# Optimization experiments

Measured on AMD Instinct MI355X. Metric: run time of the kernel, lower is better.

Reference implementation:

```python
import jax, jax.numpy as jnp
import numpy as np

B, S, D = 4, 2048, 512
H, Dh = 8, 64  # head_dim(=num heads)=8, qkv_dim(per-head)=64
SCALE = 1.0 / float(np.sqrt(Dh))


def setup_inputs() -> dict:
    key = jax.random.key(0)
    ks = jax.random.split(key, 11)
    w = 1.0 / float(np.sqrt(D))
    return {
        "x": jax.random.normal(ks[0], (B, S, D), dtype=jnp.float32),
        "mask": jax.random.randint(ks[1], (B, 1, S, S), 0, 2, dtype=jnp.int32),
        "Wq": jax.random.normal(ks[2], (D, H * Dh), dtype=jnp.float32) * w,
        "bq": jax.random.normal(ks[3], (H * Dh,), dtype=jnp.float32) * w,
        "Wk": jax.random.normal(ks[4], (D, H * Dh), dtype=jnp.float32) * w,
        "bk": jax.random.normal(ks[5], (H * Dh,), dtype=jnp.float32) * w,
        "Wv": jax.random.normal(ks[6], (D, H * Dh), dtype=jnp.float32) * w,
        "bv": jax.random.normal(ks[7], (H * Dh,), dtype=jnp.float32) * w,
        "Wo": jax.random.normal(ks[8], (H * Dh, D), dtype=jnp.float32) * w,
        "bo": jax.random.normal(ks[9], (D,), dtype=jnp.float32) * w,
    }


def reference(x, mask, Wq, bq, Wk, bk, Wv, bv, Wo, bo):
    b = x.shape[0]
    q = (x @ Wq + bq).reshape(b, S, H, Dh)
    k = (x @ Wk + bk).reshape(b, S, H, Dh)
    v = (x @ Wv + bv).reshape(b, S, H, Dh)
    # [b,h,q,k] attention scores, softmax over k
    score = jax.nn.softmax(jnp.einsum('bqhd,bkhd->bhqk', q, k) * SCALE, axis=-1)
    # faithful quirk: mask applied AFTER softmax, masked entries set to 1e-20
    score = jnp.where(mask == 1, jnp.float32(1e-20), score)
    # faithful quirk: einsum 'bvhd,bhqk->bvhd' sums score over q AND k -> [b,h] scalar per head
    s = score.sum(axis=(-2, -1))  # [b, h]
    att = v * s[:, None, :, None]  # [b, S, H, Dh]
    out = att.reshape(b, S, H * Dh) @ Wo + bo
    return out
```

## Files before the change

### kernel.cpp

```cpp
#include <hip/hip_runtime.h>
#include <cstdint>
#include <cstddef>

#define DEVINL __device__ __forceinline__

constexpr int S_ = 2048;
constexpr int D_ = 512;
constexpr int H_ = 8;
constexpr float SCALE_ = 0.125f;
constexpr float SCALE_L2E_ = 0.18033688011112f;

using short8 = __attribute__((ext_vector_type(8))) short;
using f32x4  = __attribute__((ext_vector_type(4))) float;

DEVINL unsigned short f2bf(float f){
  unsigned u = __builtin_bit_cast(unsigned, f);
  u += 0x7FFFu + ((u >> 16) & 1u);
  return (unsigned short)(u >> 16);
}
DEVINL float bf2f(unsigned short h){
  return __builtin_bit_cast(float, ((unsigned)h) << 16);
}

DEVINL float fast_exp2(float x){ return __builtin_amdgcn_exp2f(x); }

DEVINL void gload16(const void* g, void* l){
  __builtin_amdgcn_global_load_lds(
      (__attribute__((address_space(1))) void*)(g),
      (__attribute__((address_space(3))) void*)(l), 16, 0, 0);
}

__global__ __launch_bounds__(256) void prep_kernel(
    const float* __restrict__ x, unsigned short* __restrict__ xb,
    const int* __restrict__ mask, unsigned char* __restrict__ bits,
    const float* __restrict__ W0, const float* __restrict__ W1,
    const float* __restrict__ W2, const float* __restrict__ W3,
    unsigned short* __restrict__ WT)
{
  __shared__ float tile[32][33];
  const int bid = blockIdx.x, t = threadIdx.x;
  if (bid < 2048){
    int i = bid * 256 + t;
    const float* p = x + (size_t)i * 8;
    float4 a = *(const float4*)p;
    float4 b = *(const float4*)(p + 4);
    short8 o;
    o[0]=f2bf(a.x); o[1]=f2bf(a.y); o[2]=f2bf(a.z); o[3]=f2bf(a.w);
    o[4]=f2bf(b.x); o[5]=f2bf(b.y); o[6]=f2bf(b.z); o[7]=f2bf(b.w);
    *(short8*)(xb + (size_t)i*8) = o;
  } else if (bid < 4096){
    unsigned tid = (bid - 2048) * 256 + t;
    #pragma unroll
    for (int it = 0; it < 4; ++it){
      size_t bidx = (size_t)tid + (size_t)it * 524288;
      const int* p = mask + bidx * 8;
      int4 a = *(const int4*)p;
      int4 c = *(const int4*)(p + 4);
      unsigned v = (unsigned)(a.x != 0)       | ((unsigned)(a.y != 0) << 1)
                 | ((unsigned)(a.z != 0) << 2) | ((unsigned)(a.w != 0) << 3)
                 | ((unsigned)(c.x != 0) << 4) | ((unsigned)(c.y != 0) << 5)
                 | ((unsigned)(c.z != 0) << 6) | ((unsigned)(c.w != 0) << 7);
      bits[bidx] = (unsigned char)v;
    }
  } else {
    const int b2 = bid - 4096;
    const int z = b2 >> 8, r = b2 & 255;
    const float* W = (z==0) ? W0 : (z==1 ? W1 : (z==2 ? W2 : W3));
    const float scale = (z==0) ? SCALE_L2E_ : 1.0f;
    unsigned short* out = WT + (size_t)z * D_ * D_;
    const int n0 = (r & 15)*32, k0 = (r >> 4)*32;
    const int tx = t & 31, ty = t >> 5;
    #pragma unroll
    for (int j=0;j<4;j++)
      tile[ty+j*8][tx] = W[(size_t)(k0+ty+j*8)*D_ + n0+tx];
    __syncthreads();
    #pragma unroll
    for (int j=0;j<4;j++)
      out[(size_t)(n0+ty+j*8)*D_ + k0+tx] = f2bf(tile[tx][ty+j*8]*scale);
  }
}

template<typename OutT>
__global__ __launch_bounds__(256) void gemm_bt(
    const unsigned short* __restrict__ A, long long Az,
    const unsigned short* __restrict__ BT, long long Bz,
    const float* __restrict__ bias0, const float* __restrict__ bias1, const float* __restrict__ bias2,
    float bs0, float bs1, float bs2,
    OutT* __restrict__ Cp, long long Cz)
{
  __shared__ unsigned short As[128*64];
  __shared__ unsigned short Bs[128*64];
  const int z = blockIdx.z;
  const unsigned short* Ab = A + (size_t)z*Az;
  const unsigned short* Bb = BT + (size_t)z*Bz;
  const float* bias = (z==0) ? bias0 : (z==1 ? bias1 : bias2);
  const float bscale = (z==0) ? bs0 : (z==1 ? bs1 : bs2);
  OutT* C = Cp + (size_t)z*Cz;
  const int m0 = blockIdx.y*128, n0 = blockIdx.x*128;
  const int t = threadIdx.x, lane = t & 63, w = t >> 6;
  const int wr = w >> 1, wc = w & 1;
  const int g = lane >> 4, lq = lane & 15;
  f32x4 acc[4][4] = {};
  for (int kk = 0; kk < D_; kk += 64){
    #pragma unroll
    for (int p = 0; p < 4; p++){
      int o = p*4096 + t*16;
      int row = o >> 7;
      int cb  = o & 127;
      int scb = cb ^ ((row & 7) << 4);
      gload16((const char*)Ab + ((size_t)(m0+row)*D_ + kk)*2 + scb, (char*)As + o);
      gload16((const char*)Bb + ((size_t)(n0+row)*D_ + kk)*2 + scb, (char*)Bs + o);
    }
    __syncthreads();
    #pragma unroll
    for (int ks = 0; ks < 2; ks++){
      short8 af[4], bf[4];
      #pragma unroll
      for (int i = 0; i < 4; i++){
        int rowA = wr*64 + i*16 + lq;
        af[i] = *(const short8*)((const char*)As + ((rowA*128 + ks*64 + g*16) ^ ((rowA&7)<<4)));
        int rowB = wc*64 + i*16 + lq;
        bf[i] = *(const short8*)((const char*)Bs + ((rowB*128 + ks*64 + g*16) ^ ((rowB&7)<<4)));
      }
      #pragma unroll
      for (int i = 0; i < 4; i++)
        #pragma unroll
        for (int j = 0; j < 4; j++)
          acc[i][j] = __builtin_amdgcn_mfma_f32_16x16x32_bf16(af[i], bf[j], acc[i][j], 0, 0, 0);
    }
    __syncthreads();
  }
  #pragma unroll
  for (int i = 0; i < 4; i++){
    #pragma unroll
    for (int j = 0; j < 4; j++){
      int col = n0 + wc*64 + j*16 + lq;
      float bvv = bias[col]*bscale;
      #pragma unroll
      for (int r = 0; r < 4; r++){
        int row = m0 + wr*64 + i*16 + g*4 + r;
        float v = acc[i][j][r] + bvv;
        if constexpr (sizeof(OutT) == 4) C[(size_t)row*D_ + col] = (OutT)v;
        else                             C[(size_t)row*D_ + col] = (OutT)f2bf(v);
      }
    }
  }
}

__global__ __launch_bounds__(512) void attn_zm_kernel(
    const unsigned short* __restrict__ Q, const unsigned short* __restrict__ Kg,
    const unsigned* __restrict__ bitsW, float* __restrict__ Zp, float* __restrict__ Mp)
{
  __shared__ unsigned short Ks[2][128*64];
  const int bid = blockIdx.x;
  const int kz = bid & 7;
  const int qt = (bid >> 3) & 3;
  const int bh = bid >> 5;
  const int b = bh >> 3, h = bh & 7;
  const int t = threadIdx.x, lane = t & 63, w = t >> 6;
  const int g = lane >> 4, lq = lane & 15;
  const int qbase = qt*512 + w*64;

  unsigned wb[4][8];
  #pragma unroll
  for (int qs = 0; qs < 4; qs++){
    const uint4* wp = (const uint4*)(bitsW + ((size_t)(b*S_ + qbase + qs*16 + lq))*(S_/32) + kz*8);
    uint4 wA = wp[0], wB = wp[1];
    wb[qs][0]=wA.x; wb[qs][1]=wA.y; wb[qs][2]=wA.z; wb[qs][3]=wA.w;
    wb[qs][4]=wB.x; wb[qs][5]=wB.y; wb[qs][6]=wB.z; wb[qs][7]=wB.w;
  }
  short8 qf[4][2];
  #pragma unroll
  for (int qs = 0; qs < 4; qs++)
    #pragma unroll
    for (int c = 0; c < 2; c++)
      qf[qs][c] = *(const short8*)(Q + ((size_t)(b*S_ + qbase + qs*16 + lq))*D_ + h*64 + c*32 + g*8);
  __builtin_amdgcn_sched_barrier(0);

  const char* Kgb = (const char*)Kg + ((size_t)(b*S_ + kz*256))*1024 + h*128;
  #pragma unroll
  for (int p = 0; p < 2; p++){
    int o = p*8192 + t*16;
    int row = o >> 7;
    int scb = (o & 127) ^ ((row & 7) << 4);
    gload16(Kgb + (size_t)row*1024 + scb, (char*)Ks[0] + o);
  }
  #pragma unroll
  for (int p = 0; p < 2; p++){
    int o = p*8192 + t*16;
    int row = o >> 7;
    int scb = (o & 127) ^ ((row & 7) << 4);
    gload16(Kgb + (size_t)(row + 128)*1024 + scb, (char*)Ks[1] + o);
  }

  float Z[4], Mm[4];
  #pragma unroll
  for (int qs = 0; qs < 4; qs++){ Z[qs] = 0.f; Mm[qs] = 0.f; }

  asm volatile("s_waitcnt vmcnt(2)" ::: "memory");
  __builtin_amdgcn_sched_barrier(0);
  __builtin_amdgcn_s_barrier();

#define ATTN_HALF(HB, WOFF)                                                       \
  _Pragma("unroll")                                                               \
  for (int i = 0; i < 8; ++i){                                                    \
    const int row = i*16 + lq;                                                    \
    const int sw = (row & 7) << 4;                                                \
    short8 A0 = *(const short8*)((const char*)Ks[HB] + row*128 + ((g*16) ^ sw));  \
    short8 A1 = *(const short8*)((const char*)Ks[HB] + row*128 + ((64 + g*16) ^ sw)); \
    _Pragma("unroll")                                                             \
    for (int qs = 0; qs < 4; qs++){                                               \
      f32x4 d = {0.f,0.f,0.f,0.f};                                                \
      d = __builtin_amdgcn_mfma_f32_16x16x32_bf16(A0, qf[qs][0], d, 0, 0, 0);     \
      d = __builtin_amdgcn_mfma_f32_16x16x32_bf16(A1, qf[qs][1], d, 0, 0, 0);     \
      unsigned nib = wb[qs][WOFF + (i >> 1)] >> ((i & 1)*16 + g*4);               \
      _Pragma("unroll")                                                           \
      for (int r = 0; r < 4; r++){                                                \
        float p = fast_exp2(d[r]);                                                \
        Z[qs] += p;                                                               \
        Mm[qs] = fmaf((float)((nib >> r) & 1u), p, Mm[qs]);                       \
      }                                                                           \
    }                                                                             \
  }

  ATTN_HALF(0, 0)

  asm volatile("s_waitcnt vmcnt(0)" ::: "memory");
  __builtin_amdgcn_sched_barrier(0);
  __builtin_amdgcn_s_barrier();

  ATTN_HALF(1, 4)
#undef ATTN_HALF

  #pragma unroll
  for (int qs = 0; qs < 4; qs++){
    Z[qs]  += __shfl_xor(Z[qs], 16);  Mm[qs] += __shfl_xor(Mm[qs], 16);
    Z[qs]  += __shfl_xor(Z[qs], 32);  Mm[qs] += __shfl_xor(Mm[qs], 32);
  }
  if (g == 0){
    size_t base = ((size_t)(kz*32 + bh))*S_ + qbase + lq;
    #pragma unroll
    for (int qs = 0; qs < 4; qs++){
      Zp[base + qs*16] = Z[qs];
      Mp[base + qs*16] = Mm[qs];
    }
  }
}

__global__ __launch_bounds__(256) void finalize_s(const float* __restrict__ Zp,
                                                  const float* __restrict__ Mp,
                                                  float* __restrict__ sbh){
  const int bh = blockIdx.x;
  const int t = threadIdx.x;
  float acc = 0.f;
  for (int q = t; q < S_; q += 256){
    float z = 0.f, m = 0.f;
    #pragma unroll
    for (int kz = 0; kz < 8; kz++){
      size_t idx = ((size_t)(kz*32 + bh))*S_ + q;
      z += Zp[idx];
      m += Mp[idx];
    }
    acc += (z - m) / z;
  }
  #pragma unroll
  for (int m = 1; m < 64; m <<= 1) acc += __shfl_xor(acc, m);
  __shared__ float wsum[4];
  if ((t & 63) == 0) wsum[t >> 6] = acc;
  __syncthreads();
  if (t == 0) sbh[bh] = wsum[0] + wsum[1] + wsum[2] + wsum[3];
}

__global__ void scale_woT_kernel(const unsigned short* __restrict__ WoT,
                                 const float* __restrict__ sbh,
                                 unsigned short* __restrict__ outw){
  int i = blockIdx.x*256 + threadIdx.x;
  size_t e = (size_t)i * 8;
  int k = (int)(e & 511);
  int n = (int)((e >> 9) & 511);
  int b = (int)(e >> 18);
  float sv = sbh[b*H_ + (k >> 6)];
  short8 wv = *(const short8*)(WoT + (size_t)n*D_ + k);
  short8 o;
  #pragma unroll
  for (int j = 0; j < 8; j++) o[j] = (short)f2bf(bf2f((unsigned short)wv[j]) * sv);
  *(short8*)(outw + e) = o;
}

extern "C" void kernel_launch(void* const* d_in, const int* in_sizes, int n_in,
                              void* d_out, int out_size, void* d_ws, size_t ws_size,
                              hipStream_t stream) {
  (void)in_sizes; (void)n_in; (void)out_size; (void)ws_size;
  const float* x  = (const float*)d_in[0];
  const int* mask = (const int*)d_in[1];
  const float* Wq = (const float*)d_in[2];
  const float* bq = (const float*)d_in[3];
  const float* Wk = (const float*)d_in[4];
  const float* bk = (const float*)d_in[5];
  const float* Wv = (const float*)d_in[6];
  const float* bv = (const float*)d_in[7];
  const float* Wo = (const float*)d_in[8];
  const float* bo = (const float*)d_in[9];
  float* out = (float*)d_out;

  char* ws = (char*)d_ws;
  unsigned short* xb   = (unsigned short*)(ws);
  unsigned short* wT   = (unsigned short*)(ws +  8388608);
  unsigned short* woT  = (unsigned short*)(ws +  9961472);
  unsigned short* Qb   = (unsigned short*)(ws + 10485760);
  unsigned short* Kb   = (unsigned short*)(ws + 18874368);
  unsigned short* Vb   = (unsigned short*)(ws + 27262976);
  unsigned short* woST = (unsigned short*)(ws + 35651584);
  float*          sbh  = (float*)         (ws + 37748736);
  float*          Zp   = (float*)(ws);
  float*          Mp   = (float*)(ws + 2097152);
  unsigned char*  bits = (unsigned char*)(ws + 35651584);

  prep_kernel<<<5120, 256, 0, stream>>>(x, xb, mask, bits, Wq, Wk, Wv, Wo, wT);

  gemm_bt<unsigned short><<<dim3(4,64,3), 256, 0, stream>>>(
      xb, 0LL, wT, 262144LL, bq, bk, bv, SCALE_L2E_, 1.0f, 1.0f, Qb, 4194304LL);

  attn_zm_kernel<<<1024, 512, 0, stream>>>(Qb, Kb, (const unsigned*)bits, Zp, Mp);
  finalize_s<<<32, 256, 0, stream>>>(Zp, Mp, sbh);

  scale_woT_kernel<<<512, 256, 0, stream>>>(woT, sbh, woST);

  gemm_bt<float><<<dim3(4,16,4), 256, 0, stream>>>(
      Vb, 1048576LL, woST, 262144LL, bo, bo, bo, 1.0f, 1.0f, 1.0f, out, 1048576LL);
}
```

Measured before the change: 102.8 us.

## Fuse finalize with Wo scaling, swizzle GEMM blocks, remap attention grid, add setprio

Merges the per-head score reduction and the Wo-scaling step into one kernel, which removes a launch and the round trip of the sbh buffer. The QKV GEMM now uses a 1D grid whose block index is remapped so that consecutive blocks spread across XCDs. The attention kernel's block index is decoded so the key-split index is the slowest dimension. Wave priority is raised around the MFMA/exp sections. The fused finalize uses only 32 blocks to scale Wo, so that step runs with very little parallelism.

```diff
diff --git a/kernel.cpp b/kernel.cpp
--- a/kernel.cpp
+++ b/kernel.cpp
@@ -80,7 +80,7 @@
   }
 }
 
-template<typename OutT>
+template<typename OutT, bool SWZ>
 __global__ __launch_bounds__(256) void gemm_bt(
     const unsigned short* __restrict__ A, long long Az,
     const unsigned short* __restrict__ BT, long long Bz,
@@ -90,13 +90,17 @@
 {
   __shared__ unsigned short As[128*64];
   __shared__ unsigned short Bs[128*64];
-  const int z = blockIdx.z;
+  int xx, yy, z;
+  if constexpr (SWZ){
+    int i = (blockIdx.x & 7)*96 + (blockIdx.x >> 3);
+    int g = i >> 6; yy = i & 63; xx = g & 3; z = g >> 2;
+  } else { xx = blockIdx.x; yy = blockIdx.y; z = blockIdx.z; }
   const unsigned short* Ab = A + (size_t)z*Az;
   const unsigned short* Bb = BT + (size_t)z*Bz;
   const float* bias = (z==0) ? bias0 : (z==1 ? bias1 : bias2);
   const float bscale = (z==0) ? bs0 : (z==1 ? bs1 : bs2);
   OutT* C = Cp + (size_t)z*Cz;
-  const int m0 = blockIdx.y*128, n0 = blockIdx.x*128;
+  const int m0 = yy*128, n0 = xx*128;
   const int t = threadIdx.x, lane = t & 63, w = t >> 6;
   const int wr = w >> 1, wc = w & 1;
   const int g = lane >> 4, lq = lane & 15;
@@ -153,9 +157,10 @@
 {
   __shared__ unsigned short Ks[2][128*64];
   const int bid = blockIdx.x;
-  const int kz = bid & 7;
-  const int qt = (bid >> 3) & 3;
-  const int bh = bid >> 5;
+  const int kz = bid >> 7;
+  const int rr = bid & 127;
+  const int bh = rr >> 2;
+  const int qt = rr & 3;
   const int b = bh >> 3, h = bh & 7;
   const int t = threadIdx.x, lane = t & 63, w = t >> 6;
   const int g = lane >> 4, lq = lane & 15;
@@ -223,13 +228,17 @@
     }                                                                             \
   }
 
+  __builtin_amdgcn_s_setprio(1);
   ATTN_HALF(0, 0)
+  __builtin_amdgcn_s_setprio(0);
 
   asm volatile("s_waitcnt vmcnt(0)" ::: "memory");
   __builtin_amdgcn_sched_barrier(0);
   __builtin_amdgcn_s_barrier();
 
+  __builtin_amdgcn_s_setprio(1);
   ATTN_HALF(1, 4)
+  __builtin_amdgcn_s_setprio(0);
 #undef ATTN_HALF
 
   #pragma unroll
@@ -247,10 +256,11 @@
   }
 }
 
-__global__ __launch_bounds__(256) void finalize_s(const float* __restrict__ Zp,
-                                                  const float* __restrict__ Mp,
-                                                  float* __restrict__ sbh){
-  const int bh = blockIdx.x;
+__global__ __launch_bounds__(256) void finalize_scale(
+    const float* __restrict__ Zp, const float* __restrict__ Mp,
+    const unsigned short* __restrict__ woT, unsigned short* __restrict__ woST)
+{
+  const int bh = blockIdx.x, b = bh >> 3, h = bh & 7;
   const int t = threadIdx.x;
   float acc = 0.f;
   for (int q = t; q < S_; q += 256){
@@ -264,27 +274,20 @@
     acc += (z - m) / z;
   }
   #pragma unroll
-  for (int m = 1; m < 64; m <<= 1) acc += __shfl_xor(acc, m);
+  for (int mm = 1; mm < 64; mm <<= 1) acc += __shfl_xor(acc, mm);
   __shared__ float wsum[4];
   if ((t & 63) == 0) wsum[t >> 6] = acc;
   __syncthreads();
-  if (t == 0) sbh[bh] = wsum[0] + wsum[1] + wsum[2] + wsum[3];
-}
-
-__global__ void scale_woT_kernel(const unsigned short* __restrict__ WoT,
-                                 const float* __restrict__ sbh,
-                                 unsigned short* __restrict__ outw){
-  int i = blockIdx.x*256 + threadIdx.x;
-  size_t e = (size_t)i * 8;
-  int k = (int)(e & 511);
-  int n = (int)((e >> 9) & 511);
-  int b = (int)(e >> 18);
-  float sv = sbh[b*H_ + (k >> 6)];
-  short8 wv = *(const short8*)(WoT + (size_t)n*D_ + k);
-  short8 o;
-  #pragma unroll
-  for (int j = 0; j < 8; j++) o[j] = (short)f2bf(bf2f((unsigned short)wv[j]) * sv);
-  *(short8*)(outw + e) = o;
+  const float sv = wsum[0] + wsum[1] + wsum[2] + wsum[3];
+  for (int idx = t; idx < 4096; idx += 256){
+    int n = idx >> 3, kq = idx & 7;
+    size_t off = (size_t)n*D_ + h*64 + kq*8;
+    short8 wv = *(const short8*)(woT + off);
+    short8 o;
+    #pragma unroll
+    for (int j = 0; j < 8; j++) o[j] = (short)f2bf(bf2f((unsigned short)wv[j]) * sv);
+    *(short8*)(woST + (size_t)b*262144 + off) = o;
+  }
 }
 
 extern "C" void kernel_launch(void* const* d_in, const int* in_sizes, int n_in,
@@ -311,21 +314,19 @@
   unsigned short* Kb   = (unsigned short*)(ws + 18874368);
   unsigned short* Vb   = (unsigned short*)(ws + 27262976);
   unsigned short* woST = (unsigned short*)(ws + 35651584);
-  float*          sbh  = (float*)         (ws + 37748736);
   float*          Zp   = (float*)(ws);
   float*          Mp   = (float*)(ws + 2097152);
   unsigned char*  bits = (unsigned char*)(ws + 35651584);
 
   prep_kernel<<<5120, 256, 0, stream>>>(x, xb, mask, bits, Wq, Wk, Wv, Wo, wT);
 
-  gemm_bt<unsigned short><<<dim3(4,64,3), 256, 0, stream>>>(
+  gemm_bt<unsigned short, true><<<768, 256, 0, stream>>>(
       xb, 0LL, wT, 262144LL, bq, bk, bv, SCALE_L2E_, 1.0f, 1.0f, Qb, 4194304LL);
 
   attn_zm_kernel<<<1024, 512, 0, stream>>>(Qb, Kb, (const unsigned*)bits, Zp, Mp);
-  finalize_s<<<32, 256, 0, stream>>>(Zp, Mp, sbh);
-
-  scale_woT_kernel<<<512, 256, 0, stream>>>(woT, sbh, woST);
-
-  gemm_bt<float><<<dim3(4,16,4), 256, 0, stream>>>(
+
+  finalize_scale<<<32, 256, 0, stream>>>(Zp, Mp, woT, woST);
+
+  gemm_bt<float, false><<<dim3(4,16,4), 256, 0, stream>>>(
       Vb, 1048576LL, woST, 262144LL, bo, bo, bo, 1.0f, 1.0f, 1.0f, out, 1048576LL);
 }
```

New measurement: 105.2 us. 2.3% more time.
